# Optimization experiments

Measured on AMD Instinct MI355X. Metric: run time of the kernel, lower is better.

Reference implementation:

```python
import jax, jax.numpy as jnp
import numpy as np

N_WG = 256                 # waveguides per side
N_TOTAL = N_WG * N_WG      # 65536 field points
NNZ = 16 * N_TOTAL         # ~16 couplings per waveguide (Knn-banded)
PROP_DIS = 1.0


def setup_inputs() -> dict:
    key = jax.random.key(0)
    k1, k2, k3, k4, k5 = jax.random.split(key, 5)
    row_idx = jax.random.randint(k1, (NNZ,), 0, N_TOTAL, dtype=jnp.int32)
    col_idx = jax.random.randint(k2, (NNZ,), 0, N_TOTAL, dtype=jnp.int32)
    # small coupling values so the explicit Euler scheme stays stable
    A_vals = jax.random.normal(k3, (NNZ,), dtype=jnp.float32) * 0.01
    Ur0 = jax.random.normal(k4, (N_TOTAL, 1), dtype=jnp.float32)
    Ui0 = jax.random.normal(k5, (N_TOTAL, 1), dtype=jnp.float32)
    return {"A_vals": A_vals, "row_idx": row_idx, "col_idx": col_idx,
            "Ur0": Ur0, "Ui0": Ui0, "Euler_steps": 16}


def reference(A_vals, row_idx, col_idx, Ur0, Ui0, Euler_steps):
    """Euler propagation of a complex field U under sparse coupling A:
       dU/dz = i * A @ U  ->  Ur' = Ur - dz*A@Ui ; Ui' = Ui + dz*A@Ur.
       Matches gen_Euler_with_backward_devs.forward (single device block)."""
    dz = PROP_DIS / Euler_steps

    def spmm(x):  # sparse COO matmul: [n, n] @ [n, 1]
        return jax.ops.segment_sum(A_vals[:, None] * x[col_idx], row_idx,
                                   num_segments=N_TOTAL)

    def step(carry, _):
        Ur, Ui = carry
        Ur1 = Ur - dz * spmm(Ui)
        Ui1 = Ui + dz * spmm(Ur)
        return (Ur1, Ui1), None

    (Ur, Ui), _ = jax.lax.scan(step, (Ur0, Ui0), None, length=Euler_steps)
    return Ur + 1j * Ui
```

## Files before the change

### kernel.cpp

```cpp
#include <hip/hip_runtime.h>

#define N_TOTAL 65536
#define NNZ (16 * N_TOTAL)
#define EULER_STEPS 16
#define SLOTS 48
#define TB 256


__device__ __forceinline__ unsigned pack_entry(int col, float v) {
  unsigned b = __float_as_uint(v);
  unsigned r = (b + 0x7FFFu + ((b >> 16) & 1u)) & 0xFFFF0000u;
  return (unsigned)col | r;
}

__global__ __launch_bounds__(TB) void fill_ell_kernel(
    const float* __restrict__ A_vals, const int* __restrict__ row_idx,
    const int* __restrict__ col_idx, int* __restrict__ cursor,
    unsigned* __restrict__ entries) {
  int e = blockIdx.x * blockDim.x + threadIdx.x;
  if (e < NNZ) {
    int r = row_idx[e];
    int pos = atomicAdd(cursor + r, 1);
    if (pos < SLOTS)
      entries[r * SLOTS + pos] = pack_entry(col_idx[e], A_vals[e]);
  }
}


__device__ __forceinline__ void reduce4(float& sR, float& sI) {
  sR += __shfl_xor(sR, 1); sI += __shfl_xor(sI, 1);
  sR += __shfl_xor(sR, 2); sI += __shfl_xor(sI, 2);
}

__global__ __launch_bounds__(TB) void step_first_kernel(
    const int* __restrict__ cnt, const unsigned* __restrict__ entries,
    const float* __restrict__ Ur0, const float* __restrict__ Ui0,
    float2* __restrict__ Unew, float dz) {
  int tid = blockIdx.x * blockDim.x + threadIdx.x;
  int row = tid >> 2, l = tid & 3;
  if (row >= N_TOTAL) return;
  int c = cnt[row];
  if (c > SLOTS) c = SLOTS;
  const unsigned* base = entries + row * SLOTS;
  float sR = 0.0f, sI = 0.0f;
  for (int k = 2 * l; k < c; k += 8) {
    uint2 p = *(const uint2*)(base + k);
    {
      float a = __uint_as_float(p.x & 0xFFFF0000u);
      int col = (int)(p.x & 0xFFFFu);
      sR += a * Ur0[col];
      sI += a * Ui0[col];
    }
    if (k + 1 < c) {
      float a = __uint_as_float(p.y & 0xFFFF0000u);
      int col = (int)(p.y & 0xFFFFu);
      sR += a * Ur0[col];
      sI += a * Ui0[col];
    }
  }
  reduce4(sR, sI);
  if (l == 0)
    Unew[row] = make_float2(Ur0[row] - dz * sI, Ui0[row] + dz * sR);
}

__global__ __launch_bounds__(TB) void step_mid_kernel(
    const int* __restrict__ cnt, const unsigned* __restrict__ entries,
    const float2* __restrict__ Uold, float2* __restrict__ Unew, float dz) {
  int tid = blockIdx.x * blockDim.x + threadIdx.x;
  int row = tid >> 2, l = tid & 3;
  if (row >= N_TOTAL) return;
  int c = cnt[row];
  if (c > SLOTS) c = SLOTS;
  const unsigned* base = entries + row * SLOTS;
  float sR = 0.0f, sI = 0.0f;
  for (int k = 2 * l; k < c; k += 8) {
    uint2 p = *(const uint2*)(base + k);
    {
      float a = __uint_as_float(p.x & 0xFFFF0000u);
      float2 u = Uold[p.x & 0xFFFFu];
      sR += a * u.x;
      sI += a * u.y;
    }
    if (k + 1 < c) {
      float a = __uint_as_float(p.y & 0xFFFF0000u);
      float2 u = Uold[p.y & 0xFFFFu];
      sR += a * u.x;
      sI += a * u.y;
    }
  }
  reduce4(sR, sI);
  if (l == 0) {
    float2 u = Uold[row];
    Unew[row] = make_float2(u.x - dz * sI, u.y + dz * sR);
  }
}

__global__ __launch_bounds__(TB) void step_final_kernel(
    const int* __restrict__ cnt, const unsigned* __restrict__ entries,
    const float2* __restrict__ Uold, float* __restrict__ UrOut,
    float* __restrict__ UiOut, float dz) {
  int tid = blockIdx.x * blockDim.x + threadIdx.x;
  int row = tid >> 2, l = tid & 3;
  if (row >= N_TOTAL) return;
  int c = cnt[row];
  if (c > SLOTS) c = SLOTS;
  const unsigned* base = entries + row * SLOTS;
  float sR = 0.0f, sI = 0.0f;
  for (int k = 2 * l; k < c; k += 8) {
    uint2 p = *(const uint2*)(base + k);
    {
      float a = __uint_as_float(p.x & 0xFFFF0000u);
      float2 u = Uold[p.x & 0xFFFFu];
      sR += a * u.x;
      sI += a * u.y;
    }
    if (k + 1 < c) {
      float a = __uint_as_float(p.y & 0xFFFF0000u);
      float2 u = Uold[p.y & 0xFFFFu];
      sR += a * u.x;
      sI += a * u.y;
    }
  }
  reduce4(sR, sI);
  if (l == 0) {
    float2 u = Uold[row];
    UrOut[row] = u.x - dz * sI;
    UiOut[row] = u.y + dz * sR;
  }
}

extern "C" void kernel_launch(void* const* d_in, const int* in_sizes, int n_in,
                              void* d_out, int out_size, void* d_ws,
                              size_t ws_size, hipStream_t stream) {
  const float* A_vals  = (const float*)d_in[0];
  const int*   row_idx = (const int*)d_in[1];
  const int*   col_idx = (const int*)d_in[2];
  const float* Ur0     = (const float*)d_in[3];
  const float* Ui0     = (const float*)d_in[4];

  float2*   bufA    = (float2*)d_ws;
  float2*   bufB    = bufA + N_TOTAL;
  int*      cursor  = (int*)(bufB + N_TOTAL);
  unsigned* entries = (unsigned*)(cursor + N_TOTAL);

  float* UrOut = (float*)d_out;
  float* UiOut = UrOut + N_TOTAL;
  const float dz = 1.0f / (float)EULER_STEPS;

  const int gridN4  = (4 * N_TOTAL) / TB;
  const int gridNNZ = NNZ / TB;

  hipMemsetAsync(cursor, 0, N_TOTAL * sizeof(int), stream);
  fill_ell_kernel<<<gridNNZ, TB, 0, stream>>>(A_vals, row_idx, col_idx,
                                              cursor, entries);

  step_first_kernel<<<gridN4, TB, 0, stream>>>(cursor, entries, Ur0, Ui0,
                                               bufB, dz);
  for (int s = 1; s < EULER_STEPS - 1; ++s) {
    const float2* src = (s & 1) ? bufB : bufA;
    float2*       dst = (s & 1) ? bufA : bufB;
    step_mid_kernel<<<gridN4, TB, 0, stream>>>(cursor, entries, src, dst, dz);
  }
  step_final_kernel<<<gridN4, TB, 0, stream>>>(cursor, entries, bufB, UrOut,
                                               UiOut, dz);
}
```

Baseline: 269.0 us.

## Fuse ELL fill with first Euler step using per-block row ownership

Replaces the global-atomic ELL build, the memset and the first step kernel with one kernel of 128 blocks. Each block owns 512 rows, scans the full row index array, and counts slots with shared-memory atomics instead of global ones. The block then computes the first Euler step for its own rows, using two lanes per row. The cost is that every block rereads the whole 4MB row_idx array, and only 128 workgroups run, leaving many CUs idle during the fill.

```diff
diff --git a/kernel.cpp b/kernel.cpp
--- a/kernel.cpp
+++ b/kernel.cpp
@@ -5,6 +5,9 @@
 #define EULER_STEPS 16
 #define SLOTS 48
 #define TB 256
+#define OWNERS 128
+#define ROWS_PER_OWNER (N_TOTAL / OWNERS)
+#define FILLTB 1024
 
 
 __device__ __forceinline__ unsigned pack_entry(int col, float v) {
@@ -13,38 +16,45 @@
   return (unsigned)col | r;
 }
 
-__global__ __launch_bounds__(TB) void fill_ell_kernel(
+__global__ __launch_bounds__(FILLTB) void fill_step1_kernel(
     const float* __restrict__ A_vals, const int* __restrict__ row_idx,
-    const int* __restrict__ col_idx, int* __restrict__ cursor,
-    unsigned* __restrict__ entries) {
-  int e = blockIdx.x * blockDim.x + threadIdx.x;
-  if (e < NNZ) {
-    int r = row_idx[e];
-    int pos = atomicAdd(cursor + r, 1);
-    if (pos < SLOTS)
-      entries[r * SLOTS + pos] = pack_entry(col_idx[e], A_vals[e]);
+    const int* __restrict__ col_idx, const float* __restrict__ Ur0,
+    const float* __restrict__ Ui0, int* __restrict__ cnt,
+    unsigned* __restrict__ entries, float2* __restrict__ Unew, float dz) {
+  __shared__ int cur[ROWS_PER_OWNER];
+  const int bid = blockIdx.x, tid = threadIdx.x;
+  const int rlo = bid * ROWS_PER_OWNER;
+
+  for (int r = tid; r < ROWS_PER_OWNER; r += FILLTB) cur[r] = 0;
+  __syncthreads();
+
+  const int4* rows4 = (const int4*)row_idx;
+  for (int i = tid; i < NNZ / 4; i += FILLTB) {
+    int4 r4 = rows4[i];
+    int base = 4 * i;
+#pragma unroll
+    for (int c = 0; c < 4; ++c) {
+      int r = (c == 0) ? r4.x : (c == 1) ? r4.y : (c == 2) ? r4.z : r4.w;
+      if ((r >> 9) == bid) {
+        int slot = atomicAdd(&cur[r - rlo], 1);
+        if (slot < SLOTS)
+          entries[r * SLOTS + slot] =
+              pack_entry(col_idx[base + c], A_vals[base + c]);
+      }
+    }
   }
-}
+  __syncthreads();
 
+  for (int r = tid; r < ROWS_PER_OWNER; r += FILLTB) cnt[rlo + r] = cur[r];
 
-__device__ __forceinline__ void reduce4(float& sR, float& sI) {
-  sR += __shfl_xor(sR, 1); sI += __shfl_xor(sI, 1);
-  sR += __shfl_xor(sR, 2); sI += __shfl_xor(sI, 2);
-}
-
-__global__ __launch_bounds__(TB) void step_first_kernel(
-    const int* __restrict__ cnt, const unsigned* __restrict__ entries,
-    const float* __restrict__ Ur0, const float* __restrict__ Ui0,
-    float2* __restrict__ Unew, float dz) {
-  int tid = blockIdx.x * blockDim.x + threadIdx.x;
-  int row = tid >> 2, l = tid & 3;
-  if (row >= N_TOTAL) return;
-  int c = cnt[row];
+  const int lr = tid >> 1, l = tid & 1;
+  const int row = rlo + lr;
+  int c = cur[lr];
   if (c > SLOTS) c = SLOTS;
-  const unsigned* base = entries + row * SLOTS;
+  const unsigned* ebase = entries + row * SLOTS;
   float sR = 0.0f, sI = 0.0f;
-  for (int k = 2 * l; k < c; k += 8) {
-    uint2 p = *(const uint2*)(base + k);
+  for (int k = 2 * l; k < c; k += 4) {
+    uint2 p = *(const uint2*)(ebase + k);
     {
       float a = __uint_as_float(p.x & 0xFFFF0000u);
       int col = (int)(p.x & 0xFFFFu);
@@ -58,7 +68,8 @@
       sI += a * Ui0[col];
     }
   }
-  reduce4(sR, sI);
+  sR += __shfl_xor(sR, 1);
+  sI += __shfl_xor(sI, 1);
   if (l == 0)
     Unew[row] = make_float2(Ur0[row] - dz * sI, Ui0[row] + dz * sR);
 }
@@ -88,7 +99,8 @@
       sI += a * u.y;
     }
   }
-  reduce4(sR, sI);
+  sR += __shfl_xor(sR, 1); sI += __shfl_xor(sI, 1);
+  sR += __shfl_xor(sR, 2); sI += __shfl_xor(sI, 2);
   if (l == 0) {
     float2 u = Uold[row];
     Unew[row] = make_float2(u.x - dz * sI, u.y + dz * sR);
@@ -121,7 +133,8 @@
       sI += a * u.y;
     }
   }
-  reduce4(sR, sI);
+  sR += __shfl_xor(sR, 1); sI += __shfl_xor(sI, 1);
+  sR += __shfl_xor(sR, 2); sI += __shfl_xor(sI, 2);
   if (l == 0) {
     float2 u = Uold[row];
     UrOut[row] = u.x - dz * sI;
@@ -140,27 +153,23 @@
 
   float2*   bufA    = (float2*)d_ws;
   float2*   bufB    = bufA + N_TOTAL;
-  int*      cursor  = (int*)(bufB + N_TOTAL);
-  unsigned* entries = (unsigned*)(cursor + N_TOTAL);
+  int*      cnt     = (int*)(bufB + N_TOTAL);
+  unsigned* entries = (unsigned*)(cnt + N_TOTAL);
 
   float* UrOut = (float*)d_out;
   float* UiOut = UrOut + N_TOTAL;
   const float dz = 1.0f / (float)EULER_STEPS;
 
-  const int gridN4  = (4 * N_TOTAL) / TB;
-  const int gridNNZ = NNZ / TB;
+  const int gridN4 = (4 * N_TOTAL) / TB;
 
-  hipMemsetAsync(cursor, 0, N_TOTAL * sizeof(int), stream);
-  fill_ell_kernel<<<gridNNZ, TB, 0, stream>>>(A_vals, row_idx, col_idx,
-                                              cursor, entries);
+  fill_step1_kernel<<<OWNERS, FILLTB, 0, stream>>>(
+      A_vals, row_idx, col_idx, Ur0, Ui0, cnt, entries, bufB, dz);
 
-  step_first_kernel<<<gridN4, TB, 0, stream>>>(cursor, entries, Ur0, Ui0,
-                                               bufB, dz);
   for (int s = 1; s < EULER_STEPS - 1; ++s) {
     const float2* src = (s & 1) ? bufB : bufA;
     float2*       dst = (s & 1) ? bufA : bufB;
-    step_mid_kernel<<<gridN4, TB, 0, stream>>>(cursor, entries, src, dst, dz);
+    step_mid_kernel<<<gridN4, TB, 0, stream>>>(cnt, entries, src, dst, dz);
   }
-  step_final_kernel<<<gridN4, TB, 0, stream>>>(cursor, entries, bufB, UrOut,
+  step_final_kernel<<<gridN4, TB, 0, stream>>>(cnt, entries, bufB, UrOut,
                                                UiOut, dz);
 }
```

New measurement: 434.2 us. +61.4%, slower.
